# Optimization experiments

Hardware: AMD Instinct MI355X
Metric: run time of the kernel (lower is better)

## Reference

```python
import jax, jax.numpy as jnp
import numpy as np

H, W = 8192, 16384          # dna_shape = (out_features, in_features)
NUM_TRANSFORMS = 8
NUM_POINTS = 1000           # hardcoded in source
CHAOS_ITERS = 10            # hardcoded in source
B = 2048


def setup_inputs() -> dict:
    key = jax.random.key(0)
    k1, k2, k3 = jax.random.split(key, 3)
    x = jax.random.normal(k1, (B, W), dtype=jnp.float32)
    # flat IFS params: [a,b,c,d,e,f,p] per transform; scaled down so affine maps are mostly contractive
    dna_params = jax.random.normal(k2, (NUM_TRANSFORMS * 7,), dtype=jnp.float32) * 0.5
    bias = jax.random.normal(k3, (H,), dtype=jnp.float32)
    return {"x": x, "dna_params": dna_params, "bias": bias}


def reference(x, dna_params, bias):
    params = dna_params.reshape(NUM_TRANSFORMS, 7)  # (T, 7)
    # theta[t] = [[a, b, e], [c, d, f]]  -> (T, 2, 3) affine maps
    theta = jnp.stack([
        jnp.stack([params[:, 0], params[:, 1], params[:, 4]], axis=1),
        jnp.stack([params[:, 2], params[:, 3], params[:, 5]], axis=1),
    ], axis=1)

    key = jax.random.key(1)
    kp, kg = jax.random.split(key)
    points = jax.random.uniform(kp, (NUM_POINTS, 2), dtype=x.dtype) * 2.0 - 1.0  # (N, 2) in [-1, 1)
    logits = jnp.broadcast_to(params[:, 6], (NUM_POINTS, NUM_TRANSFORMS))

    # Chaos game: 10 iterations of hard gumbel-softmax transform selection + affine map
    for i in range(CHAOS_ITERS):
        g = jax.random.gumbel(jax.random.fold_in(kg, i), (NUM_POINTS, NUM_TRANSFORMS), dtype=x.dtype)
        soft = jax.nn.softmax(logits + g, axis=-1)  # tau = 1.0
        hard = jax.nn.one_hot(jnp.argmax(soft, axis=-1), NUM_TRANSFORMS, dtype=soft.dtype)
        gw = hard + soft - jax.lax.stop_gradient(soft)          # straight-through hard sample (N, T)
        t_theta = jnp.einsum('nt,trc->nrc', gw, theta)          # (N, 2, 3) per-point affine
        ph = jnp.concatenate([points, jnp.ones((NUM_POINTS, 1), dtype=points.dtype)], axis=1)  # (N, 3)
        points = jnp.einsum('nrc,nc->nr', t_theta, ph)          # (N, 2)

    # Map attractor points to matrix coordinates
    y_coords = (points[:, 1] + 1.0) * 0.5 * (H - 1)
    x_coords = (points[:, 0] + 1.0) * 0.5 * (W - 1)
    y_low = jnp.clip(jnp.floor(y_coords).astype(jnp.int32), 0, H - 2)
    y_w = y_coords - y_low.astype(y_coords.dtype)
    x_low = jnp.clip(jnp.floor(x_coords).astype(jnp.int32), 0, W - 2)
    x_w = x_coords - x_low.astype(x_coords.dtype)

    # Bilinear gather along in_features: (B, N)
    x_vals = x[:, x_low] * (1.0 - x_w) + x[:, x_low + 1] * x_w

    # Bilinear scatter-add along out_features: (B, H)
    y = jnp.zeros((x.shape[0], H), dtype=x.dtype)
    y = y.at[:, y_low].add(x_vals * (1.0 - y_w))
    y = y.at[:, y_low + 1].add(x_vals * y_w)
    return y / NUM_POINTS + bias
```

## Files before the change

kernel.cpp:

```cpp
#include <hip/hip_runtime.h>
#include <stdint.h>

#ifndef PRNG_PARTITIONABLE
#define PRNG_PARTITIONABLE 1
#endif

namespace {

constexpr int kH  = 8192;
constexpr int kW  = 16384;
constexpr int kNT = 8;
constexpr int kNP = 1000;
constexpr int kCI = 10;
constexpr int kRPB = 2;

constexpr size_t kOffRec  = 0;
constexpr size_t kOffRec2 = 16384;

typedef float floatx4 __attribute__((ext_vector_type(4)));

__device__ __forceinline__ uint32_t rotl32(uint32_t x, int n) {
  return (x << n) | (x >> (32 - n));
}

__device__ void threefry2x32(uint32_t k0, uint32_t k1, uint32_t c0, uint32_t c1,
                             uint32_t& o0, uint32_t& o1) {
  const uint32_t ks2 = k0 ^ k1 ^ 0x1BD11BDAu;
  uint32_t x0 = c0 + k0, x1 = c1 + k1;
#define TF_R(r) { x0 += x1; x1 = rotl32(x1, (r)); x1 ^= x0; }
  TF_R(13) TF_R(15) TF_R(26) TF_R(6)
  x0 += k1;  x1 += ks2 + 1u;
  TF_R(17) TF_R(29) TF_R(16) TF_R(24)
  x0 += ks2; x1 += k0 + 2u;
  TF_R(13) TF_R(15) TF_R(26) TF_R(6)
  x0 += k0;  x1 += k1 + 3u;
  TF_R(17) TF_R(29) TF_R(16) TF_R(24)
  x0 += k1;  x1 += ks2 + 4u;
  TF_R(13) TF_R(15) TF_R(26) TF_R(6)
  x0 += ks2; x1 += k0 + 5u;
#undef TF_R
  o0 = x0; o1 = x1;
}

__device__ __forceinline__ uint32_t random_bits32(uint32_t k0, uint32_t k1,
                                                  uint32_t i, uint32_t size) {
#if PRNG_PARTITIONABLE
  uint32_t o0, o1;
  threefry2x32(k0, k1, 0u , i, o0, o1);
  (void)size;
  return o0 ^ o1;
#else
  const uint32_t half = size / 2u;
  const uint32_t j = (i < half) ? i : (i - half);
  uint32_t o0, o1;
  threefry2x32(k0, k1, j, j + half, o0, o1);
  return (i < half) ? o0 : o1;
#endif
}

__device__ __forceinline__ float u01(uint32_t bits) {
  return __uint_as_float((bits >> 9) | 0x3f800000u) - 1.0f;
}

__device__ __forceinline__ int cvt_f32_i32_x86(float v) {
  if (!(v >= -2147483648.0f && v < 2147483648.0f)) return (int)0x80000000;
  return (int)v;
}

__global__ __launch_bounds__(256) void fractal_chaos(
    const float* __restrict__ dna, int4* __restrict__ rec) {
  const int gid  = blockIdx.x * blockDim.x + threadIdx.x;
  const int n    = gid >> 3;
  const int lane = gid & 7;
  if (n >= kNP) return;

  uint32_t kp0, kp1, kg0, kg1;
#if PRNG_PARTITIONABLE
  threefry2x32(0u, 1u, 0u, 0u, kp0, kp1);
  threefry2x32(0u, 1u, 0u, 1u, kg0, kg1);
#else
  uint32_t a0, a1, b0, b1;
  threefry2x32(0u, 1u, 0u, 2u, a0, a1);
  threefry2x32(0u, 1u, 1u, 3u, b0, b1);
  kp0 = a0; kp1 = b0; kg0 = a1; kg1 = b1;
#endif

  const float A  = dna[lane * 7 + 0], Bb = dna[lane * 7 + 1];
  const float C  = dna[lane * 7 + 2], D  = dna[lane * 7 + 3];
  const float E  = dna[lane * 7 + 4], F  = dna[lane * 7 + 5];
  const float P  = dna[lane * 7 + 6];

  float z[kCI];
  #pragma unroll
  for (int i = 0; i < kCI; ++i) {
    uint32_t ki0, ki1;
    threefry2x32(kg0, kg1, 0u, (uint32_t)i, ki0, ki1);
    const uint32_t bb = random_bits32(ki0, ki1, (uint32_t)(n * kNT + lane),
                                      (uint32_t)(kNP * kNT));
    const float u = fmaxf(u01(bb), 1.17549435e-38f);
    const float g = -logf(-logf(u));
    z[i] = P + g;
  }

  const uint32_t bx = random_bits32(kp0, kp1, (uint32_t)(2 * n),     2u * kNP);
  const uint32_t by = random_bits32(kp0, kp1, (uint32_t)(2 * n + 1), 2u * kNP);
  float px = u01(bx) * 2.0f - 1.0f;
  float py = u01(by) * 2.0f - 1.0f;

  #pragma unroll
  for (int i = 0; i < kCI; ++i) {
    float zb = z[i];
    int   bt = lane;
    #pragma unroll
    for (int m = 1; m < 8; m <<= 1) {
      const float zo = __shfl_xor(zb, m, 8);
      const int   to = __shfl_xor(bt, m, 8);
      if (zo > zb || (zo == zb && to < bt)) { zb = zo; bt = to; }
    }
    const float A_ = __shfl(A,  bt, 8), B_ = __shfl(Bb, bt, 8);
    const float C_ = __shfl(C,  bt, 8), D_ = __shfl(D,  bt, 8);
    const float E_ = __shfl(E,  bt, 8), F_ = __shfl(F,  bt, 8);
    const float nx = A_ * px + B_ * py + E_;
    const float ny = C_ * px + D_ * py + F_;
    px = nx; py = ny;
  }

  if (lane == 0) {
    const float xc = ((px + 1.0f) * 0.5f) * (float)(kW - 1);
    const float yc = ((py + 1.0f) * 0.5f) * (float)(kH - 1);
    int xl = cvt_f32_i32_x86(floorf(xc));
    int yl = cvt_f32_i32_x86(floorf(yc));
    xl = min(max(xl, 0), kW - 2);
    yl = min(max(yl, 0), kH - 2);
    const float xw = xc - (float)xl;
    const float yw = yc - (float)yl;
    rec[n] = make_int4(xl, __float_as_int(xw), yl, __float_as_int(yw));
  }
}

__global__ __launch_bounds__(1024) void fractal_build(
    const int4* __restrict__ rec, int4* __restrict__ rec2) {
  __shared__ uint32_t cnt[1024];
  __shared__ uint32_t seg[1024];

  const int t = threadIdx.x;
  cnt[t] = 0;
  __syncthreads();

  int4 r = make_int4(0, 0, 0, 0);
  int bx = 0;
  const bool hav = t < kNP;
  if (hav) {
    r = rec[t];
    bx = r.x >> 4;
    atomicAdd(&cnt[bx], 1u);
  }
  __syncthreads();

  seg[t] = cnt[t];
  __syncthreads();
  #pragma unroll
  for (int o = 1; o < 1024; o <<= 1) {
    uint32_t v = (t >= o) ? seg[t - o] : 0u;
    __syncthreads();
    seg[t] += v;
    __syncthreads();
  }
  cnt[t] = (t > 0) ? seg[t - 1] : 0u;
  __syncthreads();

  if (hav) {
    const uint32_t p = atomicAdd(&cnt[bx], 1u);
    rec2[p] = r;
  }
}

__global__ __launch_bounds__(1024) void fractal_apply(
    const float* __restrict__ x, const float* __restrict__ bias,
    const int4* __restrict__ rec2, float* __restrict__ out, int B) {
  __shared__ __align__(16) float acc[kRPB * kH];
  const int b0 = blockIdx.x * kRPB;
  const int nrows = min(kRPB, B - b0);
  const int tid = threadIdx.x;

  const bool havept = tid < kNP;
  int4 r = make_int4(0, 0, 0, 0);
  float v0[kRPB], v1[kRPB];
  if (havept) {
    r = rec2[tid];
    const float* xp = x + (size_t)b0 * kW + r.x;
    #pragma unroll
    for (int rI = 0; rI < kRPB; ++rI) {
      if (rI < nrows) {
        v0[rI] = xp[(size_t)rI * kW];
        v1[rI] = xp[(size_t)rI * kW + 1];
      }
    }
  }

  float4* acc4 = reinterpret_cast<float4*>(acc);
  constexpr int N4 = kRPB * kH / 4;
  for (int i = tid; i < N4; i += 1024)
    acc4[i] = make_float4(0.f, 0.f, 0.f, 0.f);
  __syncthreads();

  if (havept) {
    const float xw = __int_as_float(r.y);
    const float yw = __int_as_float(r.w);
    const float xw0 = 1.0f - xw;
    const float w0  = 1.0f - yw;
    const int yl = r.z;
    #pragma unroll
    for (int rI = 0; rI < kRPB; ++rI) {
      if (rI < nrows) {
        const float xv = v0[rI] * xw0 + v1[rI] * xw;
        atomicAdd(&acc[rI * kH + yl],     xv * w0);
        atomicAdd(&acc[rI * kH + yl + 1], xv * yw);
      }
    }
  }
  __syncthreads();

  const floatx4* __restrict__ bias4 = reinterpret_cast<const floatx4*>(bias);
  for (int i = tid; i < N4; i += 1024) {
    const int row = i >> 11;
    const int col = i & 2047;
    if (row < nrows) {
      const float4 a  = acc4[i];
      const floatx4 bi = bias4[col];
      floatx4 o;
      o.x = a.x / 1000.0f + bi.x;
      o.y = a.y / 1000.0f + bi.y;
      o.z = a.z / 1000.0f + bi.z;
      o.w = a.w / 1000.0f + bi.w;
      floatx4* dst = reinterpret_cast<floatx4*>(out + (size_t)(b0 + row) * kH);
      __builtin_nontemporal_store(o, &dst[col]);
    }
  }
}

}

extern "C" void kernel_launch(void* const* d_in, const int* in_sizes, int n_in,
                              void* d_out, int out_size, void* d_ws, size_t ws_size,
                              hipStream_t stream) {
  const float* x    = (const float*)d_in[0];
  const float* dna  = (const float*)d_in[1];
  const float* bias = (const float*)d_in[2];
  float* out = (float*)d_out;

  char* ws = (char*)d_ws;
  int4* rec  = (int4*)(ws + kOffRec);
  int4* rec2 = (int4*)(ws + kOffRec2);

  fractal_chaos<<<(kNP * 8 + 255) / 256, 256, 0, stream>>>(dna, rec);
  fractal_build<<<1, 1024, 0, stream>>>(rec, rec2);

  const int B = in_sizes[0] / kW;
  fractal_apply<<<(B + kRPB - 1) / kRPB, 1024, 0, stream>>>(x, bias, rec2,
                                                            out, B);
}
```

Baseline: 49.22 us.

## Split apply into chunked coalesced gather and per-row scatter kernels

Replaces the fused gather+scatter kernel with two kernels. The first stages 1024-column chunks of each x row into shared memory with coalesced float4 loads and computes the interpolated values for points sorted by chunk, writing them to a workspace buffer. The second accumulates each output row in shared memory and adds bias. The aim is to swap scattered global reads of x for coalesced chunk loads. The cost is an extra kernel launch, an intermediate XV buffer round-trip, and reading whole chunks even when few points fall in them, though chunks with no points are skipped.

```diff
diff --git a/kernel.cpp b/kernel.cpp
--- a/kernel.cpp
+++ b/kernel.cpp
@@ -12,10 +12,16 @@
 constexpr int kNT = 8;
 constexpr int kNP = 1000;
 constexpr int kCI = 10;
+constexpr int kCh = 16;
+constexpr int kChW = kW / kCh;
 constexpr int kRPB = 2;
 
-constexpr size_t kOffRec  = 0;
-constexpr size_t kOffRec2 = 16384;
+constexpr size_t kOffRec    = 0;
+constexpr size_t kOffRowPtr = 16384;
+constexpr size_t kOffRec2   = 16512;
+constexpr size_t kOffRec3   = 24576;
+constexpr size_t kOffXV     = 32768;
+constexpr size_t kWsNeeded  = kOffXV + (size_t)2048 * 1024 * 4;
 
 typedef float floatx4 __attribute__((ext_vector_type(4)));
 
@@ -139,83 +145,154 @@
 }
 
 __global__ __launch_bounds__(1024) void fractal_build(
-    const int4* __restrict__ rec, int4* __restrict__ rec2) {
-  __shared__ uint32_t cnt[1024];
-  __shared__ uint32_t seg[1024];
+    const int4* __restrict__ rec, uint32_t* __restrict__ rowptr,
+    uint2* __restrict__ rec2, uint2* __restrict__ rec3) {
+  __shared__ uint32_t cnt[kCh];
+  __shared__ uint32_t cur[kCh];
 
   const int t = threadIdx.x;
-  cnt[t] = 0;
+  if (t < kCh) cnt[t] = 0;
   __syncthreads();
 
   int4 r = make_int4(0, 0, 0, 0);
-  int bx = 0;
+  int ch = 0;
   const bool hav = t < kNP;
   if (hav) {
     r = rec[t];
-    bx = r.x >> 4;
-    atomicAdd(&cnt[bx], 1u);
-  }
-  __syncthreads();
-
-  seg[t] = cnt[t];
-  __syncthreads();
-  #pragma unroll
-  for (int o = 1; o < 1024; o <<= 1) {
-    uint32_t v = (t >= o) ? seg[t - o] : 0u;
-    __syncthreads();
-    seg[t] += v;
-    __syncthreads();
-  }
-  cnt[t] = (t > 0) ? seg[t - 1] : 0u;
+    ch = r.x >> 10;
+    atomicAdd(&cnt[ch], 1u);
+  }
+  __syncthreads();
+
+  if (t == 0) {
+    uint32_t run = 0;
+    #pragma unroll
+    for (int k = 0; k < kCh; ++k) {
+      rowptr[k] = run;
+      cur[k] = run;
+      run += cnt[k];
+    }
+    rowptr[kCh] = run;
+  }
   __syncthreads();
 
   if (hav) {
-    const uint32_t p = atomicAdd(&cnt[bx], 1u);
-    rec2[p] = r;
-  }
-}
-
-__global__ __launch_bounds__(1024) void fractal_apply(
+    const uint32_t p = atomicAdd(&cur[ch], 1u);
+    rec2[p] = make_uint2((uint32_t)r.x, (uint32_t)r.y);
+    rec3[p] = make_uint2((uint32_t)r.z, (uint32_t)r.w);
+  }
+}
+
+__global__ __launch_bounds__(256) void fractal_gather(
+    const float* __restrict__ x, const uint32_t* __restrict__ rowptr,
+    const uint2* __restrict__ rec2, float* __restrict__ XV) {
+  const int ch = blockIdx.x;
+  const uint32_t s = rowptr[ch], e = rowptr[ch + 1];
+  if (s == e) return;
+
+  __shared__ __align__(16) float xb[kChW];
+  const int r   = blockIdx.y;
+  const int tid = threadIdx.x;
+  const int c0  = ch * kChW;
+  const float* __restrict__ xrow = x + (size_t)r * kW;
+
+  reinterpret_cast<float4*>(xb)[tid] =
+      reinterpret_cast<const float4*>(xrow + c0)[tid];
+  __syncthreads();
+
+  float* __restrict__ xvrow = XV + (size_t)r * 1024;
+  for (uint32_t i = s + tid; i < e; i += 256) {
+    const uint2 p = rec2[i];
+    const int   xl = (int)p.x;
+    const float xw = __uint_as_float(p.y);
+    const int loc = xl - c0;
+    const float v0 = xb[loc];
+    const float v1 = (loc < kChW - 1) ? xb[loc + 1] : xrow[xl + 1];
+    xvrow[i] = v0 * (1.0f - xw) + v1 * xw;
+  }
+}
+
+__global__ __launch_bounds__(256) void fractal_scatter(
+    const float* __restrict__ XV, const uint2* __restrict__ rec3,
+    const float* __restrict__ bias, float* __restrict__ out) {
+  __shared__ __align__(16) float acc[kH];
+  const int r   = blockIdx.x;
+  const int tid = threadIdx.x;
+
+  float xv[4];
+  uint2 p[4];
+  #pragma unroll
+  for (int j = 0; j < 4; ++j) {
+    const int i = tid + j * 256;
+    if (i < kNP) {
+      xv[j] = XV[(size_t)r * 1024 + i];
+      p[j]  = rec3[i];
+    }
+  }
+
+  float4* acc4 = reinterpret_cast<float4*>(acc);
+  #pragma unroll
+  for (int j = 0; j < 8; ++j)
+    acc4[tid + j * 256] = make_float4(0.f, 0.f, 0.f, 0.f);
+  __syncthreads();
+
+  #pragma unroll
+  for (int j = 0; j < 4; ++j) {
+    const int i = tid + j * 256;
+    if (i < kNP) {
+      const int   yl = (int)p[j].x;
+      const float yw = __uint_as_float(p[j].y);
+      atomicAdd(&acc[yl],     xv[j] * (1.0f - yw));
+      atomicAdd(&acc[yl + 1], xv[j] * yw);
+    }
+  }
+  __syncthreads();
+
+  const floatx4* __restrict__ bias4 = reinterpret_cast<const floatx4*>(bias);
+  floatx4* __restrict__ out4 = reinterpret_cast<floatx4*>(out + (size_t)r * kH);
+  #pragma unroll
+  for (int j = 0; j < 8; ++j) {
+    const int g = tid + j * 256;
+    const float4 a  = acc4[g];
+    const floatx4 bi = bias4[g];
+    floatx4 o;
+    o.x = a.x / 1000.0f + bi.x;
+    o.y = a.y / 1000.0f + bi.y;
+    o.z = a.z / 1000.0f + bi.z;
+    o.w = a.w / 1000.0f + bi.w;
+    __builtin_nontemporal_store(o, &out4[g]);
+  }
+}
+
+__global__ __launch_bounds__(1024) void fractal_apply_fb(
     const float* __restrict__ x, const float* __restrict__ bias,
-    const int4* __restrict__ rec2, float* __restrict__ out, int B) {
+    const int4* __restrict__ rec, float* __restrict__ out, int B) {
   __shared__ __align__(16) float acc[kRPB * kH];
   const int b0 = blockIdx.x * kRPB;
   const int nrows = min(kRPB, B - b0);
   const int tid = threadIdx.x;
 
-  const bool havept = tid < kNP;
-  int4 r = make_int4(0, 0, 0, 0);
-  float v0[kRPB], v1[kRPB];
-  if (havept) {
-    r = rec2[tid];
-    const float* xp = x + (size_t)b0 * kW + r.x;
-    #pragma unroll
-    for (int rI = 0; rI < kRPB; ++rI) {
-      if (rI < nrows) {
-        v0[rI] = xp[(size_t)rI * kW];
-        v1[rI] = xp[(size_t)rI * kW + 1];
-      }
-    }
-  }
-
   float4* acc4 = reinterpret_cast<float4*>(acc);
   constexpr int N4 = kRPB * kH / 4;
   for (int i = tid; i < N4; i += 1024)
     acc4[i] = make_float4(0.f, 0.f, 0.f, 0.f);
   __syncthreads();
 
-  if (havept) {
+  if (tid < kNP) {
+    const int4 r = rec[tid];
+    const int   xl = r.x;
     const float xw = __int_as_float(r.y);
+    const int   yl = r.z;
     const float yw = __int_as_float(r.w);
     const float xw0 = 1.0f - xw;
     const float w0  = 1.0f - yw;
-    const int yl = r.z;
+    const float* xp = x + (size_t)b0 * kW + xl;
     #pragma unroll
     for (int rI = 0; rI < kRPB; ++rI) {
       if (rI < nrows) {
-        const float xv = v0[rI] * xw0 + v1[rI] * xw;
-        atomicAdd(&acc[rI * kH + yl],     xv * w0);
-        atomicAdd(&acc[rI * kH + yl + 1], xv * yw);
+        const float xvv = xp[(size_t)rI * kW] * xw0 + xp[(size_t)rI * kW + 1] * xw;
+        atomicAdd(&acc[rI * kH + yl],     xvv * w0);
+        atomicAdd(&acc[rI * kH + yl + 1], xvv * yw);
       }
     }
   }
@@ -250,13 +327,22 @@
   float* out = (float*)d_out;
 
   char* ws = (char*)d_ws;
-  int4* rec  = (int4*)(ws + kOffRec);
-  int4* rec2 = (int4*)(ws + kOffRec2);
+  int4*     rec    = (int4*)(ws + kOffRec);
+  uint32_t* rowptr = (uint32_t*)(ws + kOffRowPtr);
+  uint2*    rec2   = (uint2*)(ws + kOffRec2);
+  uint2*    rec3   = (uint2*)(ws + kOffRec3);
+  float*    XV     = (float*)(ws + kOffXV);
+
+  const int B = in_sizes[0] / kW;
 
   fractal_chaos<<<(kNP * 8 + 255) / 256, 256, 0, stream>>>(dna, rec);
-  fractal_build<<<1, 1024, 0, stream>>>(rec, rec2);
-
-  const int B = in_sizes[0] / kW;
-  fractal_apply<<<(B + kRPB - 1) / kRPB, 1024, 0, stream>>>(x, bias, rec2,
-                                                            out, B);
-}
+
+  if (ws_size >= kWsNeeded && B == 2048) {
+    fractal_build<<<1, 1024, 0, stream>>>(rec, rowptr, rec2, rec3);
+    fractal_gather<<<dim3(kCh, B), 256, 0, stream>>>(x, rowptr, rec2, XV);
+    fractal_scatter<<<B, 256, 0, stream>>>(XV, rec3, bias, out);
+  } else {
+    fractal_apply_fb<<<(B + kRPB - 1) / kRPB, 1024, 0, stream>>>(x, bias, rec,
+                                                                 out, B);
+  }
+}
```

After: 66.69 us. 1.35x slower.
